# Optimization experiments

Hardware: AMD Instinct MI355X
Metric: run time of the kernel (lower is better)

Reference implementation:

```python
import jax, jax.numpy as jnp
import numpy as np
from jax import lax

BN_EPS = 1e-5
LN_EPS = 1e-5
EPS = 1e-6


def _bn(x, g, b, m, v):
    inv = g / jnp.sqrt(v + BN_EPS)
    return (x - m[None, :, None, None]) * inv[None, :, None, None] + b[None, :, None, None]


def _conv1x1(x, w, b=None):
    y = jnp.einsum('bchw,oc->bohw', x, w)
    if b is not None:
        y = y + b[None, :, None, None]
    return y


def _conv2d(x, w, pad_h, pad_w):
    return lax.conv_general_dilated(x, w, (1, 1), [(pad_h, pad_h), (pad_w, pad_w)],
                                    dimension_numbers=('NCHW', 'OIHW', 'NCHW'))


def _haar_dwt(x):
    # Haar analysis, stride-2: pure 2x2 add/sub arithmetic (H, W assumed even).
    B, C, H, W = x.shape
    xb = x.reshape(B, C, H // 2, 2, W // 2, 2)
    x00 = xb[:, :, :, 0, :, 0]; x01 = xb[:, :, :, 0, :, 1]
    x10 = xb[:, :, :, 1, :, 0]; x11 = xb[:, :, :, 1, :, 1]
    LL = 0.5 * (x00 + x01 + x10 + x11)
    LH = 0.5 * (-x00 + x01 - x10 + x11)
    HL = 0.5 * (-x00 - x01 + x10 + x11)
    HH = 0.5 * (x00 - x01 - x10 + x11)
    return LH, HL, HH, LL


def _haar_idwt(LH, HL, HH, LL):
    # Matches conv_transpose2d(stride=2) with the same Haar kernels.
    x00 = 0.5 * (LL - LH - HL + HH); x01 = 0.5 * (LL + LH - HL - HH)
    x10 = 0.5 * (LL - LH + HL - HH); x11 = 0.5 * (LL + LH + HL + HH)
    B, C, h, w = LL.shape
    top = jnp.stack([x00, x01], axis=-1)  # (B,C,h,w,2)
    bot = jnp.stack([x10, x11], axis=-1)
    y = jnp.stack([top, bot], axis=3)     # (B,C,h,2,w,2)
    return y.reshape(B, C, 2 * h, 2 * w)


def _soft_threshold(x, thr):
    return jnp.sign(x) * jax.nn.relu(jnp.abs(x) - thr)


def _forward(x, red_w, red_bias, red_bn_g, red_bn_b, red_bn_m, red_bn_v,
             gct_fc1_w, gct_fc1_b, gct_ln_g, gct_ln_b, gct_fc2_w, gct_fc2_b,
             rel_h_w, rel_h_b, rel_h_bn_g, rel_h_bn_b, rel_h_bn_m, rel_h_bn_v,
             rel_v_w, rel_v_b, rel_v_bn_g, rel_v_bn_b, rel_v_bn_m, rel_v_bn_v,
             rel_fus_w, rel_fus_b, hw_theta, hw_fuse_w, hw_fc_w, hw_fc_b,
             sf_w, sf_b, sf_bn_g, sf_bn_b, sf_bn_m, sf_bn_v, fin_w, fin_b):
    B, C, H, W = x.shape
    split = C // 2  # alpha = 0.5
    identity = x[:, :split]
    gate = x[:, split:]
    r = jax.nn.relu(_bn(_conv1x1(gate, red_w, red_bias), red_bn_g, red_bn_b, red_bn_m, red_bn_v))
    # --- GCT stream: GAP -> Linear -> LayerNorm -> ReLU -> Linear -> sigmoid gate ---
    ctx = r.mean(axis=(2, 3))                      # (B,Cr)
    h1 = ctx @ gct_fc1_w.T + gct_fc1_b
    mu = h1.mean(-1, keepdims=True)
    var = ((h1 - mu) ** 2).mean(-1, keepdims=True)
    h1 = (h1 - mu) / jnp.sqrt(var + LN_EPS) * gct_ln_g + gct_ln_b
    w_gct = jax.nn.sigmoid(jax.nn.relu(h1) @ gct_fc2_w.T + gct_fc2_b)
    gct_out = r * w_gct[:, :, None, None]
    # --- Rel stream: anisotropic pool -> conv/BN/ReLU -> bilinear(size-1 axis == broadcast) ---
    hf = _conv2d(r.mean(axis=2, keepdims=True), rel_h_w, 0, 1) + rel_h_b[None, :, None, None]
    hf = jax.nn.relu(_bn(hf, rel_h_bn_g, rel_h_bn_b, rel_h_bn_m, rel_h_bn_v))
    hf = jnp.broadcast_to(hf, (B, hf.shape[1], H, W))
    vf = _conv2d(r.mean(axis=3, keepdims=True), rel_v_w, 1, 0) + rel_v_b[None, :, None, None]
    vf = jax.nn.relu(_bn(vf, rel_v_bn_g, rel_v_bn_b, rel_v_bn_m, rel_v_bn_v))
    vf = jnp.broadcast_to(vf, (B, vf.shape[1], H, W))
    rel_w_map = jax.nn.sigmoid(_conv1x1(jnp.concatenate([hf, vf], axis=1), rel_fus_w, rel_fus_b))
    rel_out = r * rel_w_map
    # --- HWFE / wavelet attention ---
    LH, HL, HH, LL = _haar_dwt(r)
    t = jax.nn.sigmoid(hw_theta)                   # (3,Cr,1,1)
    m_LH = jnp.abs(LH).mean(axis=(2, 3), keepdims=True) + EPS
    m_HL = jnp.abs(HL).mean(axis=(2, 3), keepdims=True) + EPS
    m_HH = jnp.abs(HH).mean(axis=(2, 3), keepdims=True) + EPS
    LH_h = _soft_threshold(LH, t[0][None] * m_LH)
    HL_h = _soft_threshold(HL, t[1][None] * m_HL)
    HH_h = _soft_threshold(HH, t[2][None] * m_HH)
    fused = _conv1x1(jnp.concatenate([LH_h, HL_h, HH_h], axis=1), hw_fuse_w)
    X_re = _haar_idwt(LH_h, HL_h, fused, LL)       # note: fused sits in HH slot, as in source
    gap = X_re.mean(axis=(2, 3)) @ hw_fc_w.T + hw_fc_b
    attn = jax.nn.softmax(gap, axis=1)
    hwfe_out = r * attn[:, :, None, None]
    # --- stream fusion + gating ---
    interaction = gct_out * rel_out + hwfe_out
    gate_weight = jax.nn.sigmoid(_bn(_conv1x1(interaction, sf_w, sf_b), sf_bn_g, sf_bn_b, sf_bn_m, sf_bn_v))
    out = jnp.concatenate([identity, gate * gate_weight], axis=1)
    return _conv1x1(out, fin_w, fin_b)


def setup_inputs() -> dict:
    key = jax.random.key(0)
    ks = jax.random.split(key, 20)
    B, C, H, W = 16, 512, 64, 64
    Cg = C // 2           # gate channels = 256
    Cr = 16               # max(4, 256 // 16)
    Ch = Cr // 2          # 8
    Hd = max(1, Cr // 4)  # 4
    f = lambda k, s: jax.random.normal(k, s, jnp.float32) * 0.05
    return dict(
        x=jax.random.normal(ks[0], (B, C, H, W), jnp.float32),
        red_w=f(ks[1], (Cr, Cg)), red_bias=f(ks[2], (Cr,)),
        red_bn_g=jnp.ones((Cr,)), red_bn_b=jnp.zeros((Cr,)),
        red_bn_m=jnp.zeros((Cr,)), red_bn_v=jnp.ones((Cr,)),
        gct_fc1_w=f(ks[3], (Hd, Cr)), gct_fc1_b=f(ks[4], (Hd,)),
        gct_ln_g=jnp.ones((Hd,)), gct_ln_b=jnp.zeros((Hd,)),
        gct_fc2_w=f(ks[5], (Cr, Hd)), gct_fc2_b=f(ks[6], (Cr,)),
        rel_h_w=f(ks[7], (Ch, Cr, 1, 3)), rel_h_b=f(ks[8], (Ch,)),
        rel_h_bn_g=jnp.ones((Ch,)), rel_h_bn_b=jnp.zeros((Ch,)),
        rel_h_bn_m=jnp.zeros((Ch,)), rel_h_bn_v=jnp.ones((Ch,)),
        rel_v_w=f(ks[9], (Ch, Cr, 3, 1)), rel_v_b=f(ks[10], (Ch,)),
        rel_v_bn_g=jnp.ones((Ch,)), rel_v_bn_b=jnp.zeros((Ch,)),
        rel_v_bn_m=jnp.zeros((Ch,)), rel_v_bn_v=jnp.ones((Ch,)),
        rel_fus_w=f(ks[11], (Cr, 2 * Ch)), rel_fus_b=f(ks[12], (Cr,)),
        hw_theta=f(ks[13], (3, Cr, 1, 1)), hw_fuse_w=f(ks[14], (Cr, 3 * Cr)),
        hw_fc_w=f(ks[15], (Cr, Cr)), hw_fc_b=f(ks[16], (Cr,)),
        sf_w=f(ks[17], (Cg, Cr)), sf_b=f(ks[18], (Cg,)),
        sf_bn_g=jnp.ones((Cg,)), sf_bn_b=jnp.zeros((Cg,)),
        sf_bn_m=jnp.zeros((Cg,)), sf_bn_v=jnp.ones((Cg,)),
        fin_w=f(ks[19], (C, C)), fin_b=jnp.zeros((C,)),
    )


def reference(x, red_w, red_bias, red_bn_g, red_bn_b, red_bn_m, red_bn_v,
              gct_fc1_w, gct_fc1_b, gct_ln_g, gct_ln_b, gct_fc2_w, gct_fc2_b,
              rel_h_w, rel_h_b, rel_h_bn_g, rel_h_bn_b, rel_h_bn_m, rel_h_bn_v,
              rel_v_w, rel_v_b, rel_v_bn_g, rel_v_bn_b, rel_v_bn_m, rel_v_bn_v,
              rel_fus_w, rel_fus_b, hw_theta, hw_fuse_w, hw_fc_w, hw_fc_b,
              sf_w, sf_b, sf_bn_g, sf_bn_b, sf_bn_m, sf_bn_v, fin_w, fin_b):
    return _forward(x, red_w, red_bias, red_bn_g, red_bn_b, red_bn_m, red_bn_v,
                    gct_fc1_w, gct_fc1_b, gct_ln_g, gct_ln_b, gct_fc2_w, gct_fc2_b,
                    rel_h_w, rel_h_b, rel_h_bn_g, rel_h_bn_b, rel_h_bn_m, rel_h_bn_v,
                    rel_v_w, rel_v_b, rel_v_bn_g, rel_v_bn_b, rel_v_bn_m, rel_v_bn_v,
                    rel_fus_w, rel_fus_b, hw_theta, hw_fuse_w, hw_fc_w, hw_fc_b,
                    sf_w, sf_b, sf_bn_g, sf_bn_b, sf_bn_m, sf_bn_v, fin_w, fin_b)
```

## Files before the change

### kernel.cpp

```cpp
#include <hip/hip_runtime.h>
#include <cstdint>

typedef uint16_t u16;
typedef uint32_t u32;
typedef uint64_t u64;
typedef __attribute__((ext_vector_type(4))) float f32x4;
typedef __attribute__((ext_vector_type(8))) short bf16x8;

__device__ __forceinline__ u16 f2bf(float f) {
  union { float f; u32 i; } u; u.f = f;
  u32 r = u.i + 0x7FFFu + ((u.i >> 16) & 1u);
  return (u16)(r >> 16);
}
__device__ __forceinline__ float sigm(float x) { return 1.f / (1.f + __expf(-x)); }

__global__ __launch_bounds__(256) void k0_pack(
    const float* __restrict__ fw, u16* __restrict__ fwb)
{
  int i = blockIdx.x * 256 + threadIdx.x;
  f32x4 v = ((const f32x4*)fw)[i];
  u64 p = (u64)f2bf(v[0]) | ((u64)f2bf(v[1]) << 16) |
          ((u64)f2bf(v[2]) << 32) | ((u64)f2bf(v[3]) << 48);
  ((u64*)fwb)[i] = p;
}

__global__ __launch_bounds__(256) void k1_reduce(
    const float* __restrict__ x, const float* __restrict__ rw, const float* __restrict__ rb,
    const float* __restrict__ bg, const float* __restrict__ bb, const float* __restrict__ bm,
    const float* __restrict__ bv, float* __restrict__ r)
{
  __shared__ __align__(16) float wl[256][16];
  __shared__ float bl[16];
  __shared__ float sl[16];
  int t = threadIdx.x;
  if (t < 16) {
    float s = bg[t] * rsqrtf(bv[t] + 1e-5f);
    sl[t] = s;
    bl[t] = (rb[t] - bm[t]) * s + bb[t];
  }
  __syncthreads();
  for (int i = 0; i < 16; ++i) {
    int flat = i * 256 + t;
    int co = flat >> 8, c = flat & 255;
    wl[c][co] = rw[co * 256 + c] * sl[co];
  }
  __syncthreads();
  int p = blockIdx.x * 256 + t;
  int b = p >> 12, pp = p & 4095;
  const float* gsrc = x + ((size_t)(b * 512 + 256)) * 4096 + pp;
  float acc[16];
#pragma unroll
  for (int co = 0; co < 16; ++co) acc[co] = bl[co];
#pragma unroll 4
  for (int c = 0; c < 256; ++c) {
    float g = gsrc[(size_t)c * 4096];
    const f32x4* wr = (const f32x4*)(&wl[c][0]);
    f32x4 a0 = wr[0], a1 = wr[1], a2 = wr[2], a3 = wr[3];
    acc[0]  += g * a0[0]; acc[1]  += g * a0[1]; acc[2]  += g * a0[2]; acc[3]  += g * a0[3];
    acc[4]  += g * a1[0]; acc[5]  += g * a1[1]; acc[6]  += g * a1[2]; acc[7]  += g * a1[3];
    acc[8]  += g * a2[0]; acc[9]  += g * a2[1]; acc[10] += g * a2[2]; acc[11] += g * a2[3];
    acc[12] += g * a3[0]; acc[13] += g * a3[1]; acc[14] += g * a3[2]; acc[15] += g * a3[3];
  }
  float* rd = r + ((size_t)b * 16) * 4096 + pp;
#pragma unroll
  for (int co = 0; co < 16; ++co) rd[(size_t)co * 4096] = fmaxf(acc[co], 0.f);
}

__global__ __launch_bounds__(256) void k2_means(
    const float* __restrict__ r, float* __restrict__ cm, float* __restrict__ rm,
    float* __restrict__ ctx)
{
  __shared__ __align__(16) float tile[64][68];
  int bc = blockIdx.x, t = threadIdx.x;
  const float* src = r + (size_t)bc * 4096;
#pragma unroll
  for (int i = 0; i < 4; ++i) {
    int off = (i * 256 + t) * 4;
    int row = off >> 6, col = off & 63;
    f32x4 v = *(const f32x4*)(src + off);
    *(f32x4*)&tile[row][col] = v;
  }
  __syncthreads();
  int wv = t >> 6, lane = t & 63;
  if (wv == 0) {
    float s = 0.f;
    for (int h = 0; h < 64; ++h) s += tile[h][lane];
    cm[bc * 64 + lane] = s * (1.f / 64.f);
    float tot = s;
#pragma unroll
    for (int m = 32; m; m >>= 1) tot += __shfl_xor(tot, m, 64);
    if (lane == 0) ctx[bc] = tot * (1.f / 4096.f);
  } else if (wv == 1) {
    float s = 0.f;
    for (int w0 = 0; w0 < 64; ++w0) s += tile[lane][(w0 + lane) & 63];
    rm[bc * 64 + lane] = s * (1.f / 64.f);
  }
}

__global__ __launch_bounds__(256) void k3a_gct(
    const float* __restrict__ ctx,
    const float* f1w, const float* f1b, const float* lng, const float* lnb,
    const float* f2w, const float* f2b, const float* fcw, const float* fcb,
    float* __restrict__ wgct, float* __restrict__ attn)
{
  __shared__ float cl[256];
  __shared__ float gl[256];
  int t = threadIdx.x;
  cl[t] = ctx[t];
  __syncthreads();
  int b = t >> 4, c = t & 15;
  const float* cb = &cl[b * 16];
  float a[4];
#pragma unroll
  for (int j = 0; j < 4; ++j) {
    float s = f1b[j];
    for (int i = 0; i < 16; ++i) s += cb[i] * f1w[j * 16 + i];
    a[j] = s;
  }
  float mu = 0.25f * (a[0] + a[1] + a[2] + a[3]);
  float var = 0.f;
#pragma unroll
  for (int j = 0; j < 4; ++j) { float d = a[j] - mu; var += d * d; }
  var *= 0.25f;
  float inv = rsqrtf(var + 1e-5f);
#pragma unroll
  for (int j = 0; j < 4; ++j)
    a[j] = fmaxf((a[j] - mu) * inv * lng[j] + lnb[j], 0.f);
  float s2 = f2b[c];
#pragma unroll
  for (int j = 0; j < 4; ++j) s2 += a[j] * f2w[c * 4 + j];
  wgct[t] = sigm(s2);
  float g = fcb[c];
  for (int i = 0; i < 16; ++i) g += cb[i] * fcw[c * 16 + i];
  gl[t] = g;
  __syncthreads();
  const float* gb = &gl[b * 16];
  float mx = -1e30f;
  for (int i = 0; i < 16; ++i) mx = fmaxf(mx, gb[i]);
  float den = 0.f;
  for (int i = 0; i < 16; ++i) den += __expf(gb[i] - mx);
  attn[t] = __expf(g - mx) / den;
}

__global__ __launch_bounds__(64) void k3b_rel(
    const float* __restrict__ cm, const float* __restrict__ rm,
    const float* hw, const float* hb, const float* hbg, const float* hbb, const float* hbm, const float* hbv,
    const float* vw, const float* vb_, const float* vbg, const float* vbb, const float* vbm, const float* vbv,
    const float* fw, const float* fb, float* __restrict__ hfc, float* __restrict__ vfc)
{
  __shared__ float cml[16][64], rml[16][64];
  int b = blockIdx.x, t = threadIdx.x;
  for (int i = 0; i < 16; ++i) {
    cml[i][t] = cm[(b * 16 + i) * 64 + t];
    rml[i][t] = rm[(b * 16 + i) * 64 + t];
  }
  __syncthreads();
  float hf[8], vf[8];
  for (int o = 0; o < 8; ++o) {
    float sh = 0.f, sv = 0.f;
    for (int ci = 0; ci < 16; ++ci) {
#pragma unroll
      for (int kk = 0; kk < 3; ++kk) {
        int q = t + kk - 1;
        bool ok = (q >= 0 && q < 64);
        int qi = ok ? q : 0;
        float xh = ok ? cml[ci][qi] : 0.f;
        float xv = ok ? rml[ci][qi] : 0.f;
        sh += hw[(o * 16 + ci) * 3 + kk] * xh;
        sv += vw[(o * 16 + ci) * 3 + kk] * xv;
      }
    }
    float s1 = hbg[o] * rsqrtf(hbv[o] + 1e-5f);
    hf[o] = fmaxf((sh + hb[o] - hbm[o]) * s1 + hbb[o], 0.f);
    float s2 = vbg[o] * rsqrtf(vbv[o] + 1e-5f);
    vf[o] = fmaxf((sv + vb_[o] - vbm[o]) * s2 + vbb[o], 0.f);
  }
  for (int o = 0; o < 16; ++o) {
    float sh = fb[o], sv = 0.f;
#pragma unroll
    for (int c = 0; c < 8; ++c) {
      sh += fw[o * 16 + c] * hf[c];
      sv += fw[o * 16 + 8 + c] * vf[c];
    }
    hfc[(b * 16 + o) * 64 + t] = sh;
    vfc[(b * 16 + o) * 64 + t] = sv;
  }
}

__global__ __launch_bounds__(256) void k4_pack(
    const float* __restrict__ x, const float* __restrict__ r,
    const float* __restrict__ wgct, const float* __restrict__ attn,
    const float* __restrict__ hfc, const float* __restrict__ vfc,
    const float* sfw, const float* sfb, const float* sg, const float* sb_,
    const float* sm, const float* sv, u16* __restrict__ P)
{
  __shared__ float inter[16][64];
  __shared__ __align__(16) float wsf[256][16];
  __shared__ float bsf[256];
  __shared__ float wg[16], at[16], vfh[16];
  __shared__ __align__(16) u16 t2[64][258];
  int bid = blockIdx.x;
  int b = bid >> 6, h = bid & 63;
  int t = threadIdx.x;

  for (int i = 0; i < 16; ++i) {
    int flat = i * 256 + t;
    int c = flat >> 4, q = flat & 15;
    f32x4 v = *(const f32x4*)(x + ((size_t)(b * 512 + c)) * 4096 + h * 64 + q * 4);
#pragma unroll
    for (int j = 0; j < 4; ++j) t2[q * 4 + j][c] = f2bf(v[j]);
  }
  if (t < 16) {
    wg[t] = wgct[b * 16 + t];
    at[t] = attn[b * 16 + t];
    vfh[t] = vfc[(b * 16 + t) * 64 + h];
  }
  {
    int o = t;
    float s = sg[o] * rsqrtf(sv[o] + 1e-5f);
    bsf[o] = (sfb[o] - sm[o]) * s + sb_[o];
#pragma unroll
    for (int k2 = 0; k2 < 16; ++k2) wsf[o][k2] = sfw[o * 16 + k2] * s;
  }
  __syncthreads();
  for (int i = 0; i < 32; ++i) {
    int flat = i * 256 + t;
    int wr = flat >> 7, cd = flat & 127;
    u32 d = *(const u32*)((const char*)t2 + wr * 516 + cd * 4);
    ((u32*)(P + ((size_t)(b * 4096 + h * 64 + wr)) * 512))[cd] = d;
  }
  for (int i = 0; i < 4; ++i) {
    int idx = i * 256 + t;
    int k = idx >> 6, w = idx & 63;
    float rv = r[((size_t)(b * 16 + k)) * 4096 + h * 64 + w];
    float rel = sigm(hfc[(b * 16 + k) * 64 + w] + vfh[k]);
    inter[k][w] = rv * rv * wg[k] * rel + rv * at[k];
  }
  __syncthreads();
  {
    int w = t & 63, og = t >> 6;
    float iv[16];
#pragma unroll
    for (int k2 = 0; k2 < 16; ++k2) iv[k2] = inter[k2][w];
    const float* gsrc = x + ((size_t)(b * 512 + 256)) * 4096 + h * 64 + w;
    for (int j = 0; j < 64; ++j) {
      int o = og * 64 + j;
      const f32x4* wr = (const f32x4*)(&wsf[o][0]);
      f32x4 w0 = wr[0], w1 = wr[1], w2 = wr[2], w3 = wr[3];
      float dot = bsf[o];
      dot += iv[0] * w0[0] + iv[1] * w0[1] + iv[2] * w0[2] + iv[3] * w0[3];
      dot += iv[4] * w1[0] + iv[5] * w1[1] + iv[6] * w1[2] + iv[7] * w1[3];
      dot += iv[8] * w2[0] + iv[9] * w2[1] + iv[10] * w2[2] + iv[11] * w2[3];
      dot += iv[12] * w3[0] + iv[13] * w3[1] + iv[14] * w3[2] + iv[15] * w3[3];
      float gwv = sigm(dot);
      float gv = gsrc[(size_t)o * 4096];
      t2[w][o] = f2bf(gv * gwv);
    }
  }
  __syncthreads();
  for (int i = 0; i < 32; ++i) {
    int flat = i * 256 + t;
    int wr = flat >> 7, cd = flat & 127;
    u32 d = *(const u32*)((const char*)t2 + wr * 516 + cd * 4);
    ((u32*)(P + ((size_t)(b * 4096 + h * 64 + wr)) * 512 + 256))[cd] = d;
  }
}

__global__ __launch_bounds__(512, 4) void k5_gemm(
    const u16* __restrict__ P, const u16* __restrict__ fwb,
    const float* __restrict__ fb, float* __restrict__ out)
{
  __shared__ __align__(16) u16 A[64 * 528];
  int bid = blockIdx.x;
  int b = bid >> 6, h = bid & 63;
  int t = threadIdx.x;
  int lane = t & 63, wv = t >> 6;
  int fr = lane & 15, quad = lane >> 4;

  const u16* Pb = P + (size_t)bid * 64 * 512;
#pragma unroll
  for (int i = 0; i < 8; ++i) {
    int f = i * 512 + t;
    int row = f >> 6, cf = f & 63;
    bf16x8 v = *(const bf16x8*)(Pb + (size_t)row * 512 + cf * 8);
    *(bf16x8*)(A + row * 528 + cf * 8) = v;
  }

  int n0w = wv * 64;
  f32x4 acc[4][4];
#pragma unroll
  for (int j = 0; j < 4; ++j) {
    float bvv = fb[n0w + j * 16 + fr];
    f32x4 b4 = {bvv, bvv, bvv, bvv};
#pragma unroll
    for (int i = 0; i < 4; ++i) acc[i][j] = b4;
  }
  __syncthreads();

  const u16* Bp = fwb + (size_t)(n0w + fr) * 512 + quad * 8;
  for (int kb = 0; kb < 16; ++kb) {
    int c0 = kb * 32 + quad * 8;
    bf16x8 af[4], bfr[4];
#pragma unroll
    for (int i = 0; i < 4; ++i)
      af[i] = *(const bf16x8*)(A + (i * 16 + fr) * 528 + c0);
#pragma unroll
    for (int j = 0; j < 4; ++j)
      bfr[j] = *(const bf16x8*)(Bp + (size_t)(j * 16) * 512 + kb * 32);
#pragma unroll
    for (int j = 0; j < 4; ++j)
#pragma unroll
      for (int i = 0; i < 4; ++i)
        acc[i][j] = __builtin_amdgcn_mfma_f32_16x16x32_bf16(af[i], bfr[j], acc[i][j], 0, 0, 0);
  }

  float* ob = out + ((size_t)(b * 512 + n0w + fr)) * 4096 + h * 64 + quad * 4;
#pragma unroll
  for (int j = 0; j < 4; ++j)
#pragma unroll
    for (int i = 0; i < 4; ++i)
      *(f32x4*)(ob + (size_t)(j * 16) * 4096 + i * 16) = acc[i][j];
}

__global__ __launch_bounds__(256) void k45_fused(
    const float* __restrict__ x, const float* __restrict__ r,
    const float* __restrict__ wgct, const float* __restrict__ attn,
    const float* __restrict__ hfc, const float* __restrict__ vfc,
    const float* sfw, const float* sfb, const float* sg, const float* sb_,
    const float* sm, const float* sv,
    const u16* __restrict__ fwb, const float* __restrict__ fb,
    float* __restrict__ out)
{
  __shared__ __align__(16) char region0[67584];
  __shared__ __align__(16) float wsf[256][16];
  __shared__ float inter[16][64];
  __shared__ float bsf[256];
  __shared__ float wg[16], at[16], vfh[16];
  u16* A = (u16*)region0;
  float* Dsh = (float*)region0;

  int bid = blockIdx.x;
  int b = bid >> 6, h = bid & 63;
  int t = threadIdx.x;

  for (int i = 0; i < 16; ++i) {
    int flat = i * 256 + t;
    int c = flat >> 4, q = flat & 15;
    f32x4 v = *(const f32x4*)(x + ((size_t)(b * 512 + c)) * 4096 + h * 64 + q * 4);
#pragma unroll
    for (int j = 0; j < 4; ++j) A[(q * 4 + j) * 520 + c] = f2bf(v[j]);
  }
  if (t < 16) {
    wg[t] = wgct[b * 16 + t];
    at[t] = attn[b * 16 + t];
    vfh[t] = vfc[(b * 16 + t) * 64 + h];
  }
  {
    int o = t;
    float s = sg[o] * rsqrtf(sv[o] + 1e-5f);
    bsf[o] = (sfb[o] - sm[o]) * s + sb_[o];
#pragma unroll
    for (int k2 = 0; k2 < 16; ++k2) wsf[o][k2] = sfw[o * 16 + k2] * s;
  }
  __syncthreads();
  for (int i = 0; i < 4; ++i) {
    int idx = i * 256 + t;
    int k = idx >> 6, w = idx & 63;
    float rv = r[((size_t)(b * 16 + k)) * 4096 + h * 64 + w];
    float rel = sigm(hfc[(b * 16 + k) * 64 + w] + vfh[k]);
    inter[k][w] = rv * rv * wg[k] * rel + rv * at[k];
  }
  __syncthreads();
  {
    int w = t & 63, og = t >> 6;
    float iv[16];
#pragma unroll
    for (int k2 = 0; k2 < 16; ++k2) iv[k2] = inter[k2][w];
    const float* gsrc = x + ((size_t)(b * 512 + 256)) * 4096 + h * 64 + w;
    for (int j = 0; j < 64; ++j) {
      int o = og * 64 + j;
      const f32x4* wr = (const f32x4*)(&wsf[o][0]);
      f32x4 w0 = wr[0], w1 = wr[1], w2 = wr[2], w3 = wr[3];
      float dot = bsf[o];
      dot += iv[0] * w0[0] + iv[1] * w0[1] + iv[2] * w0[2] + iv[3] * w0[3];
      dot += iv[4] * w1[0] + iv[5] * w1[1] + iv[6] * w1[2] + iv[7] * w1[3];
      dot += iv[8] * w2[0] + iv[9] * w2[1] + iv[10] * w2[2] + iv[11] * w2[3];
      dot += iv[12] * w3[0] + iv[13] * w3[1] + iv[14] * w3[2] + iv[15] * w3[3];
      float gwv = sigm(dot);
      float gv = gsrc[(size_t)o * 4096];
      A[w * 520 + 256 + o] = f2bf(gv * gwv);
    }
  }
  __syncthreads();

  int lane = t & 63, wv = t >> 6;
  int fr = lane & 15, quad = lane >> 4;
  int n0w = wv * 128;
  f32x4 acc[4][8];
#pragma unroll
  for (int j = 0; j < 8; ++j) {
    float bvv = fb[n0w + j * 16 + fr];
    f32x4 b4 = {bvv, bvv, bvv, bvv};
#pragma unroll
    for (int i = 0; i < 4; ++i) acc[i][j] = b4;
  }
  for (int kb = 0; kb < 16; ++kb) {
    int c0 = kb * 32 + quad * 8;
    bf16x8 af[4];
#pragma unroll
    for (int i = 0; i < 4; ++i)
      af[i] = *(const bf16x8*)(A + (i * 16 + fr) * 520 + c0);
#pragma unroll
    for (int j = 0; j < 8; ++j) {
      bf16x8 bfr = *(const bf16x8*)(fwb + (size_t)(n0w + j * 16 + fr) * 512 + c0);
#pragma unroll
      for (int i = 0; i < 4; ++i)
        acc[i][j] = __builtin_amdgcn_mfma_f32_16x16x32_bf16(af[i], bfr, acc[i][j], 0, 0, 0);
    }
  }
  for (int half = 0; half < 2; ++half) {
    __syncthreads();
    if ((wv >> 1) == half) {
#pragma unroll
      for (int j = 0; j < 8; ++j) {
        int nl = n0w - half * 256 + j * 16 + fr;
#pragma unroll
        for (int i = 0; i < 4; ++i)
#pragma unroll
          for (int rg = 0; rg < 4; ++rg)
            Dsh[nl * 66 + i * 16 + quad * 4 + rg] = acc[i][j][rg];
      }
    }
    __syncthreads();
    for (int it = 0; it < 64; ++it) {
      int flat = it * 256 + t;
      int nl = flat >> 6, md = flat & 63;
      float d = Dsh[nl * 66 + md];
      out[((size_t)(b * 512 + half * 256 + nl)) * 4096 + h * 64 + md] = d;
    }
  }
}

extern "C" void kernel_launch(void* const* d_in, const int* in_sizes, int n_in,
                              void* d_out, int out_size, void* d_ws, size_t ws_size,
                              hipStream_t stream) {
  const float* x      = (const float*)d_in[0];
  const float* red_w  = (const float*)d_in[1];
  const float* red_b  = (const float*)d_in[2];
  const float* rbg    = (const float*)d_in[3];
  const float* rbb    = (const float*)d_in[4];
  const float* rbm    = (const float*)d_in[5];
  const float* rbv    = (const float*)d_in[6];
  const float* f1w    = (const float*)d_in[7];
  const float* f1b    = (const float*)d_in[8];
  const float* lng    = (const float*)d_in[9];
  const float* lnb    = (const float*)d_in[10];
  const float* f2w    = (const float*)d_in[11];
  const float* f2b    = (const float*)d_in[12];
  const float* rhw    = (const float*)d_in[13];
  const float* rhb    = (const float*)d_in[14];
  const float* rhbg   = (const float*)d_in[15];
  const float* rhbb   = (const float*)d_in[16];
  const float* rhbm   = (const float*)d_in[17];
  const float* rhbv   = (const float*)d_in[18];
  const float* rvw    = (const float*)d_in[19];
  const float* rvb    = (const float*)d_in[20];
  const float* rvbg   = (const float*)d_in[21];
  const float* rvbb   = (const float*)d_in[22];
  const float* rvbm   = (const float*)d_in[23];
  const float* rvbv   = (const float*)d_in[24];
  const float* fusw   = (const float*)d_in[25];
  const float* fusb   = (const float*)d_in[26];
  const float* fcw    = (const float*)d_in[29];
  const float* fcb    = (const float*)d_in[30];
  const float* sfw    = (const float*)d_in[31];
  const float* sfb    = (const float*)d_in[32];
  const float* sbg    = (const float*)d_in[33];
  const float* sbb    = (const float*)d_in[34];
  const float* sbm    = (const float*)d_in[35];
  const float* sbv    = (const float*)d_in[36];
  const float* finw   = (const float*)d_in[37];
  const float* finb   = (const float*)d_in[38];
  float* out = (float*)d_out;

  char* ws = (char*)d_ws;
  size_t off = 0;
  float* r   = (float*)(ws + off); off += (size_t)16 * 16 * 4096 * 4;
  u16*   fwb = (u16*)(ws + off);   off += (size_t)512 * 512 * 2;
  float* cm  = (float*)(ws + off); off += 65536;
  float* rm  = (float*)(ws + off); off += 65536;
  float* ctx = (float*)(ws + off); off += 1024;
  float* wg  = (float*)(ws + off); off += 1024;
  float* at  = (float*)(ws + off); off += 1024;
  float* hfc = (float*)(ws + off); off += 65536;
  float* vfc = (float*)(ws + off); off += 65536;
  u16*   P   = (u16*)(ws + off);
  size_t need = off + (size_t)65536 * 512 * 2;
  bool split = (ws_size >= need);

  k0_pack<<<256, 256, 0, stream>>>(finw, fwb);
  k1_reduce<<<256, 256, 0, stream>>>(x, red_w, red_b, rbg, rbb, rbm, rbv, r);
  k2_means<<<256, 256, 0, stream>>>(r, cm, rm, ctx);
  k3a_gct<<<1, 256, 0, stream>>>(ctx, f1w, f1b, lng, lnb, f2w, f2b, fcw, fcb, wg, at);
  k3b_rel<<<16, 64, 0, stream>>>(cm, rm, rhw, rhb, rhbg, rhbb, rhbm, rhbv,
                                 rvw, rvb, rvbg, rvbb, rvbm, rvbv, fusw, fusb, hfc, vfc);
  if (split) {
    k4_pack<<<1024, 256, 0, stream>>>(x, r, wg, at, hfc, vfc,
                                      sfw, sfb, sbg, sbb, sbm, sbv, P);
    k5_gemm<<<1024, 512, 0, stream>>>(P, fwb, finb, out);
  } else {
    k45_fused<<<1024, 256, 0, stream>>>(x, r, wg, at, hfc, vfc,
                                        sfw, sfb, sbg, sbb, sbm, sbv, fwb, finb, out);
  }
}
```

Baseline: 464.2 us.

## Fuse gating/pack stage into the bf16 MFMA GEMM, dropping the P intermediate

```diff
diff --git a/kernel.cpp b/kernel.cpp
--- a/kernel.cpp
+++ b/kernel.cpp
@@ -187,105 +187,86 @@
   }
 }
 
-__global__ __launch_bounds__(256) void k4_pack(
+__global__ __launch_bounds__(512, 4) void k45_v2(
     const float* __restrict__ x, const float* __restrict__ r,
     const float* __restrict__ wgct, const float* __restrict__ attn,
     const float* __restrict__ hfc, const float* __restrict__ vfc,
-    const float* sfw, const float* sfb, const float* sg, const float* sb_,
-    const float* sm, const float* sv, u16* __restrict__ P)
-{
-  __shared__ float inter[16][64];
-  __shared__ __align__(16) float wsf[256][16];
-  __shared__ float bsf[256];
-  __shared__ float wg[16], at[16], vfh[16];
-  __shared__ __align__(16) u16 t2[64][258];
+    const float* __restrict__ sfw, const float* __restrict__ sfb,
+    const float* __restrict__ sg, const float* __restrict__ sb_,
+    const float* __restrict__ sbm, const float* __restrict__ sbv,
+    const u16* __restrict__ fwb, const float* __restrict__ fb,
+    float* __restrict__ out)
+{
+  __shared__ __align__(16) u16 A[64 * 528];
+  __shared__ float wgs[16], ats[16], vfhs[16];
+  char* Ab = (char*)A;
+
   int bid = blockIdx.x;
   int b = bid >> 6, h = bid & 63;
   int t = threadIdx.x;
 
-  for (int i = 0; i < 16; ++i) {
-    int flat = i * 256 + t;
-    int c = flat >> 4, q = flat & 15;
-    f32x4 v = *(const f32x4*)(x + ((size_t)(b * 512 + c)) * 4096 + h * 64 + q * 4);
-#pragma unroll
-    for (int j = 0; j < 4; ++j) t2[q * 4 + j][c] = f2bf(v[j]);
-  }
   if (t < 16) {
-    wg[t] = wgct[b * 16 + t];
-    at[t] = attn[b * 16 + t];
-    vfh[t] = vfc[(b * 16 + t) * 64 + h];
-  }
-  {
+    wgs[t]  = wgct[b * 16 + t];
+    ats[t]  = attn[b * 16 + t];
+    vfhs[t] = vfc[(b * 16 + t) * 64 + h];
+  }
+  if (t < 256) {
     int o = t;
-    float s = sg[o] * rsqrtf(sv[o] + 1e-5f);
-    bsf[o] = (sfb[o] - sm[o]) * s + sb_[o];
-#pragma unroll
-    for (int k2 = 0; k2 < 16; ++k2) wsf[o][k2] = sfw[o * 16 + k2] * s;
-  }
-  __syncthreads();
-  for (int i = 0; i < 32; ++i) {
-    int flat = i * 256 + t;
-    int wr = flat >> 7, cd = flat & 127;
-    u32 d = *(const u32*)((const char*)t2 + wr * 516 + cd * 4);
-    ((u32*)(P + ((size_t)(b * 4096 + h * 64 + wr)) * 512))[cd] = d;
-  }
-  for (int i = 0; i < 4; ++i) {
-    int idx = i * 256 + t;
+    float s = sg[o] * rsqrtf(sbv[o] + 1e-5f);
+    float* wrow = (float*)(Ab + (o & 63) * 1056 + 512 + (o >> 6) * 64);
+#pragma unroll
+    for (int k2 = 0; k2 < 16; ++k2) wrow[k2] = sfw[o * 16 + k2] * s;
+    *(float*)(Ab + (o & 63) * 1056 + 768 + (o >> 6) * 4) =
+        (sfb[o] - sbm[o]) * s + sb_[o];
+  }
+  __syncthreads();
+
+#pragma unroll
+  for (int i = 0; i < 2; ++i) {
+    int idx = i * 512 + t;
     int k = idx >> 6, w = idx & 63;
     float rv = r[((size_t)(b * 16 + k)) * 4096 + h * 64 + w];
-    float rel = sigm(hfc[(b * 16 + k) * 64 + w] + vfh[k]);
-    inter[k][w] = rv * rv * wg[k] * rel + rv * at[k];
-  }
-  __syncthreads();
+    float rel = sigm(hfc[(b * 16 + k) * 64 + w] + vfhs[k]);
+    *(float*)(Ab + w * 1056 + 784 + k * 4) =
+        rv * rv * wgs[k] * rel + rv * ats[k];
+  }
+  __syncthreads();
+
   {
     int w = t & 63, og = t >> 6;
     float iv[16];
 #pragma unroll
-    for (int k2 = 0; k2 < 16; ++k2) iv[k2] = inter[k2][w];
+    for (int k2 = 0; k2 < 16; ++k2)
+      iv[k2] = *(const float*)(Ab + w * 1056 + 784 + k2 * 4);
     const float* gsrc = x + ((size_t)(b * 512 + 256)) * 4096 + h * 64 + w;
-    for (int j = 0; j < 64; ++j) {
-      int o = og * 64 + j;
-      const f32x4* wr = (const f32x4*)(&wsf[o][0]);
+    for (int j = 0; j < 32; ++j) {
+      int o = og * 32 + j;
+      const f32x4* wr = (const f32x4*)(Ab + (o & 63) * 1056 + 512 + (o >> 6) * 64);
       f32x4 w0 = wr[0], w1 = wr[1], w2 = wr[2], w3 = wr[3];
-      float dot = bsf[o];
-      dot += iv[0] * w0[0] + iv[1] * w0[1] + iv[2] * w0[2] + iv[3] * w0[3];
-      dot += iv[4] * w1[0] + iv[5] * w1[1] + iv[6] * w1[2] + iv[7] * w1[3];
-      dot += iv[8] * w2[0] + iv[9] * w2[1] + iv[10] * w2[2] + iv[11] * w2[3];
+      float dot = *(const float*)(Ab + (o & 63) * 1056 + 768 + (o >> 6) * 4);
+      dot += iv[0]  * w0[0] + iv[1]  * w0[1] + iv[2]  * w0[2] + iv[3]  * w0[3];
+      dot += iv[4]  * w1[0] + iv[5]  * w1[1] + iv[6]  * w1[2] + iv[7]  * w1[3];
+      dot += iv[8]  * w2[0] + iv[9]  * w2[1] + iv[10] * w2[2] + iv[11] * w2[3];
       dot += iv[12] * w3[0] + iv[13] * w3[1] + iv[14] * w3[2] + iv[15] * w3[3];
       float gwv = sigm(dot);
       float gv = gsrc[(size_t)o * 4096];
-      t2[w][o] = f2bf(gv * gwv);
+      A[w * 528 + o] = f2bf(gv * gwv);
     }
   }
   __syncthreads();
-  for (int i = 0; i < 32; ++i) {
-    int flat = i * 256 + t;
-    int wr = flat >> 7, cd = flat & 127;
-    u32 d = *(const u32*)((const char*)t2 + wr * 516 + cd * 4);
-    ((u32*)(P + ((size_t)(b * 4096 + h * 64 + wr)) * 512 + 256))[cd] = d;
-  }
-}
-
-__global__ __launch_bounds__(512, 4) void k5_gemm(
-    const u16* __restrict__ P, const u16* __restrict__ fwb,
-    const float* __restrict__ fb, float* __restrict__ out)
-{
-  __shared__ __align__(16) u16 A[64 * 528];
-  int bid = blockIdx.x;
-  int b = bid >> 6, h = bid & 63;
-  int t = threadIdx.x;
+
+#pragma unroll
+  for (int i = 0; i < 8; ++i) {
+    int flat = i * 512 + t;
+    int c = flat >> 4, q = flat & 15;
+    f32x4 v = *(const f32x4*)(x + ((size_t)(b * 512 + c)) * 4096 + h * 64 + q * 4);
+#pragma unroll
+    for (int j = 0; j < 4; ++j) A[(q * 4 + j) * 528 + 256 + c] = f2bf(v[j]);
+  }
+  __syncthreads();
+
   int lane = t & 63, wv = t >> 6;
   int fr = lane & 15, quad = lane >> 4;
-
-  const u16* Pb = P + (size_t)bid * 64 * 512;
-#pragma unroll
-  for (int i = 0; i < 8; ++i) {
-    int f = i * 512 + t;
-    int row = f >> 6, cf = f & 63;
-    bf16x8 v = *(const bf16x8*)(Pb + (size_t)row * 512 + cf * 8);
-    *(bf16x8*)(A + row * 528 + cf * 8) = v;
-  }
-
   int n0w = wv * 64;
   f32x4 acc[4][4];
 #pragma unroll
@@ -295,18 +276,17 @@
 #pragma unroll
     for (int i = 0; i < 4; ++i) acc[i][j] = b4;
   }
-  __syncthreads();
-
   const u16* Bp = fwb + (size_t)(n0w + fr) * 512 + quad * 8;
   for (int kb = 0; kb < 16; ++kb) {
     int c0 = kb * 32 + quad * 8;
+    int kbb = kb ^ 8;
     bf16x8 af[4], bfr[4];
 #pragma unroll
     for (int i = 0; i < 4; ++i)
       af[i] = *(const bf16x8*)(A + (i * 16 + fr) * 528 + c0);
 #pragma unroll
     for (int j = 0; j < 4; ++j)
-      bfr[j] = *(const bf16x8*)(Bp + (size_t)(j * 16) * 512 + kb * 32);
+      bfr[j] = *(const bf16x8*)(Bp + (size_t)(j * 16) * 512 + kbb * 32);
 #pragma unroll
     for (int j = 0; j < 4; ++j)
 #pragma unroll
@@ -320,125 +300,6 @@
 #pragma unroll
     for (int i = 0; i < 4; ++i)
       *(f32x4*)(ob + (size_t)(j * 16) * 4096 + i * 16) = acc[i][j];
-}
-
-__global__ __launch_bounds__(256) void k45_fused(
-    const float* __restrict__ x, const float* __restrict__ r,
-    const float* __restrict__ wgct, const float* __restrict__ attn,
-    const float* __restrict__ hfc, const float* __restrict__ vfc,
-    const float* sfw, const float* sfb, const float* sg, const float* sb_,
-    const float* sm, const float* sv,
-    const u16* __restrict__ fwb, const float* __restrict__ fb,
-    float* __restrict__ out)
-{
-  __shared__ __align__(16) char region0[67584];
-  __shared__ __align__(16) float wsf[256][16];
-  __shared__ float inter[16][64];
-  __shared__ float bsf[256];
-  __shared__ float wg[16], at[16], vfh[16];
-  u16* A = (u16*)region0;
-  float* Dsh = (float*)region0;
-
-  int bid = blockIdx.x;
-  int b = bid >> 6, h = bid & 63;
-  int t = threadIdx.x;
-
-  for (int i = 0; i < 16; ++i) {
-    int flat = i * 256 + t;
-    int c = flat >> 4, q = flat & 15;
-    f32x4 v = *(const f32x4*)(x + ((size_t)(b * 512 + c)) * 4096 + h * 64 + q * 4);
-#pragma unroll
-    for (int j = 0; j < 4; ++j) A[(q * 4 + j) * 520 + c] = f2bf(v[j]);
-  }
-  if (t < 16) {
-    wg[t] = wgct[b * 16 + t];
-    at[t] = attn[b * 16 + t];
-    vfh[t] = vfc[(b * 16 + t) * 64 + h];
-  }
-  {
-    int o = t;
-    float s = sg[o] * rsqrtf(sv[o] + 1e-5f);
-    bsf[o] = (sfb[o] - sm[o]) * s + sb_[o];
-#pragma unroll
-    for (int k2 = 0; k2 < 16; ++k2) wsf[o][k2] = sfw[o * 16 + k2] * s;
-  }
-  __syncthreads();
-  for (int i = 0; i < 4; ++i) {
-    int idx = i * 256 + t;
-    int k = idx >> 6, w = idx & 63;
-    float rv = r[((size_t)(b * 16 + k)) * 4096 + h * 64 + w];
-    float rel = sigm(hfc[(b * 16 + k) * 64 + w] + vfh[k]);
-    inter[k][w] = rv * rv * wg[k] * rel + rv * at[k];
-  }
-  __syncthreads();
-  {
-    int w = t & 63, og = t >> 6;
-    float iv[16];
-#pragma unroll
-    for (int k2 = 0; k2 < 16; ++k2) iv[k2] = inter[k2][w];
-    const float* gsrc = x + ((size_t)(b * 512 + 256)) * 4096 + h * 64 + w;
-    for (int j = 0; j < 64; ++j) {
-      int o = og * 64 + j;
-      const f32x4* wr = (const f32x4*)(&wsf[o][0]);
-      f32x4 w0 = wr[0], w1 = wr[1], w2 = wr[2], w3 = wr[3];
-      float dot = bsf[o];
-      dot += iv[0] * w0[0] + iv[1] * w0[1] + iv[2] * w0[2] + iv[3] * w0[3];
-      dot += iv[4] * w1[0] + iv[5] * w1[1] + iv[6] * w1[2] + iv[7] * w1[3];
-      dot += iv[8] * w2[0] + iv[9] * w2[1] + iv[10] * w2[2] + iv[11] * w2[3];
-      dot += iv[12] * w3[0] + iv[13] * w3[1] + iv[14] * w3[2] + iv[15] * w3[3];
-      float gwv = sigm(dot);
-      float gv = gsrc[(size_t)o * 4096];
-      A[w * 520 + 256 + o] = f2bf(gv * gwv);
-    }
-  }
-  __syncthreads();
-
-  int lane = t & 63, wv = t >> 6;
-  int fr = lane & 15, quad = lane >> 4;
-  int n0w = wv * 128;
-  f32x4 acc[4][8];
-#pragma unroll
-  for (int j = 0; j < 8; ++j) {
-    float bvv = fb[n0w + j * 16 + fr];
-    f32x4 b4 = {bvv, bvv, bvv, bvv};
-#pragma unroll
-    for (int i = 0; i < 4; ++i) acc[i][j] = b4;
-  }
-  for (int kb = 0; kb < 16; ++kb) {
-    int c0 = kb * 32 + quad * 8;
-    bf16x8 af[4];
-#pragma unroll
-    for (int i = 0; i < 4; ++i)
-      af[i] = *(const bf16x8*)(A + (i * 16 + fr) * 520 + c0);
-#pragma unroll
-    for (int j = 0; j < 8; ++j) {
-      bf16x8 bfr = *(const bf16x8*)(fwb + (size_t)(n0w + j * 16 + fr) * 512 + c0);
-#pragma unroll
-      for (int i = 0; i < 4; ++i)
-        acc[i][j] = __builtin_amdgcn_mfma_f32_16x16x32_bf16(af[i], bfr, acc[i][j], 0, 0, 0);
-    }
-  }
-  for (int half = 0; half < 2; ++half) {
-    __syncthreads();
-    if ((wv >> 1) == half) {
-#pragma unroll
-      for (int j = 0; j < 8; ++j) {
-        int nl = n0w - half * 256 + j * 16 + fr;
-#pragma unroll
-        for (int i = 0; i < 4; ++i)
-#pragma unroll
-          for (int rg = 0; rg < 4; ++rg)
-            Dsh[nl * 66 + i * 16 + quad * 4 + rg] = acc[i][j][rg];
-      }
-    }
-    __syncthreads();
-    for (int it = 0; it < 64; ++it) {
-      int flat = it * 256 + t;
-      int nl = flat >> 6, md = flat & 63;
-      float d = Dsh[nl * 66 + md];
-      out[((size_t)(b * 512 + half * 256 + nl)) * 4096 + h * 64 + md] = d;
-    }
-  }
 }
 
 extern "C" void kernel_launch(void* const* d_in, const int* in_sizes, int n_in,
@@ -494,9 +355,6 @@
   float* at  = (float*)(ws + off); off += 1024;
   float* hfc = (float*)(ws + off); off += 65536;
   float* vfc = (float*)(ws + off); off += 65536;
-  u16*   P   = (u16*)(ws + off);
-  size_t need = off + (size_t)65536 * 512 * 2;
-  bool split = (ws_size >= need);
 
   k0_pack<<<256, 256, 0, stream>>>(finw, fwb);
   k1_reduce<<<256, 256, 0, stream>>>(x, red_w, red_b, rbg, rbb, rbm, rbv, r);
@@ -504,12 +362,6 @@
   k3a_gct<<<1, 256, 0, stream>>>(ctx, f1w, f1b, lng, lnb, f2w, f2b, fcw, fcb, wg, at);
   k3b_rel<<<16, 64, 0, stream>>>(cm, rm, rhw, rhb, rhbg, rhbb, rhbm, rhbv,
                                  rvw, rvb, rvbg, rvbb, rvbm, rvbv, fusw, fusb, hfc, vfc);
-  if (split) {
-    k4_pack<<<1024, 256, 0, stream>>>(x, r, wg, at, hfc, vfc,
-                                      sfw, sfb, sbg, sbb, sbm, sbv, P);
-    k5_gemm<<<1024, 512, 0, stream>>>(P, fwb, finb, out);
-  } else {
-    k45_fused<<<1024, 256, 0, stream>>>(x, r, wg, at, hfc, vfc,
-                                        sfw, sfb, sbg, sbb, sbm, sbv, fwb, finb, out);
-  }
-}
+  k45_v2<<<1024, 512, 0, stream>>>(x, r, wg, at, hfc, vfc,
+                                   sfw, sfb, sbg, sbb, sbm, sbv, fwb, finb, out);
+}
```

Result: faster. 440.4 us (-5.1%).
